# Kernel tuning notes

Hardware: AMD Instinct MI355X
Metric: run time of the kernel (lower is better)

The kernel has to match this reference:

```python
import jax, jax.numpy as jnp
import numpy as np

B, S, IN, H, C = 4, 1024, 1024, 256, 8

def setup_inputs() -> dict:
    key = jax.random.key(0)
    ks = jax.random.split(key, 9)
    scale_in = 1.0 / np.sqrt(IN)
    scale_h2 = 1.0 / np.sqrt(2 * H)
    return {
        "seq_feats": jax.random.normal(ks[0], (B, S, IN), dtype=jnp.float32),
        "U": jax.random.normal(ks[1], (H, C, H), dtype=jnp.float32) * 0.02,
        "W_weight": jax.random.uniform(ks[2], (C, 2 * H), minval=-scale_h2, maxval=scale_h2, dtype=jnp.float32),
        "W_bias": jax.random.uniform(ks[3], (C,), minval=-scale_h2, maxval=scale_h2, dtype=jnp.float32),
        "start_w": jax.random.uniform(ks[4], (H, IN), minval=-scale_in, maxval=scale_in, dtype=jnp.float32),
        "start_b": jax.random.uniform(ks[5], (H,), minval=-scale_in, maxval=scale_in, dtype=jnp.float32),
        "end_w": jax.random.uniform(ks[6], (H, IN), minval=-scale_in, maxval=scale_in, dtype=jnp.float32),
        "end_b": jax.random.uniform(ks[7], (H,), minval=-scale_in, maxval=scale_in, dtype=jnp.float32),
    }

def reference(seq_feats, U, W_weight, W_bias, start_w, start_b, end_w, end_b):
    # Hs, He: [b, s, h]
    Hs = jnp.einsum('bsi,hi->bsh', seq_feats, start_w) + start_b
    He = jnp.einsum('bsi,hi->bsh', seq_feats, end_w) + end_b
    # biaffine: [b, s, e, c]
    biaff = jnp.einsum('bsh,hcg,beg->bsec', Hs, U, He)
    # Linear over concat([Hs_repeat, He_repeat]) == split-weight broadcast sum
    Ws, We = W_weight[:, :256], W_weight[:, 256:]
    lin = (jnp.einsum('bsh,ch->bsc', Hs, Ws)[:, :, None, :]
           + jnp.einsum('beh,ch->bec', He, We)[:, None, :, :]
           + W_bias)
    return biaff + lin
```

## Files before the change

kernel.cpp:

```cpp
#include <hip/hip_runtime.h>
#include <stdint.h>


#define BDIM 256

typedef float f32x4 __attribute__((ext_vector_type(4)));
typedef __bf16 bf16x8 __attribute__((ext_vector_type(8)));
typedef unsigned int u32;
typedef unsigned short u16;
typedef const __attribute__((address_space(1))) u32* gas_ptr;
typedef __attribute__((address_space(3))) u32* las_ptr;

static __device__ __forceinline__ void load_lds16(const void* g, void* l) {
  __builtin_amdgcn_global_load_lds((gas_ptr)g, (las_ptr)l, 16, 0, 0);
}

static __device__ __forceinline__ u16 f32_to_bf16(float f) {
  union { float f; u32 u; } v; v.f = f;
  u32 r = v.u + 0x7FFFu + ((v.u >> 16) & 1u);
  return (u16)(r >> 16);
}
static __device__ __forceinline__ float bf16lo_to_f32(u32 u) {
  union { u32 u; float f; } v; v.u = u << 16;
  return v.f;
}
static __device__ __forceinline__ float bf16hi_to_f32(u32 u) {
  union { u32 u; float f; } v; v.u = u & 0xFFFF0000u;
  return v.f;
}

#define K3_LDSA(b) ((b) * 32768)
#define K3_LDSB(b) ((b) * 32768 + 16384)

#define STG(dstofs, src, srow, ld, kt)                                         \
  load_lds16((src) + (size_t)((srow) + (tid >> 3)) * (ld) + (kt) +             \
                 (((tid & 7) ^ ((tid >> 3) & 7)) << 3),                        \
             &lds[(dstofs) + tid * 8])

#define STG_A(b, mh, t) do {                                                   \
    STG(K3_LDSA(b) + (mh) * 4096,       Ag, m0 + (mh) * 64,       256, (t)*64);\
    STG(K3_LDSA(b) + ((mh)+2) * 4096,   Ag, m0 + 128 + (mh) * 64, 256, (t)*64);\
  } while (0)

#define STG_B(b, h, t) do {                                                    \
    STG(K3_LDSB(b) + (2*(h)) * 4096,    Bgz, n0 + (h) * 128,      512, (t)*64);\
    STG(K3_LDSB(b) + (2*(h)+1) * 4096,  Bgz, n0 + (h) * 128 + 64, 512, (t)*64);\
  } while (0)

#define RD_A(b, mh)                                                            \
  _Pragma("unroll")                                                            \
  for (int mi = 0; mi < 4; ++mi) {                                             \
    const int r = wr * 128 + (mh) * 64 + mi * 16 + rA;                         \
    _Pragma("unroll")                                                          \
    for (int ks = 0; ks < 2; ++ks)                                             \
      aF[mi][ks] = *reinterpret_cast<const bf16x8*>(                           \
          &lds[K3_LDSA(b) + r * 64 + ((((ks << 2) | kq) ^ (rA & 7)) << 3)]);   \
  }

#define RD_B(b)                                                                \
  _Pragma("unroll")                                                            \
  for (int nh = 0; nh < 2; ++nh)                                               \
  _Pragma("unroll")                                                            \
  for (int ni = 0; ni < 2; ++ni) {                                             \
    const int r = wc * 64 + nh * 32 + ni * 16 + rA;                            \
    _Pragma("unroll")                                                          \
    for (int ks = 0; ks < 2; ++ks)                                             \
      bF[nh][ni][ks] = *reinterpret_cast<const bf16x8*>(                       \
          &lds[K3_LDSB(b) + r * 64 + ((((ks << 2) | kq) ^ (rA & 7)) << 3)]);   \
  }

#define MFMA_Q(mh, nh)                                                         \
  __builtin_amdgcn_s_setprio(1);                                               \
  _Pragma("unroll")                                                            \
  for (int mi = 0; mi < 4; ++mi)                                               \
  _Pragma("unroll")                                                            \
  for (int ni = 0; ni < 2; ++ni)                                               \
  _Pragma("unroll")                                                            \
  for (int ks = 0; ks < 2; ++ks)                                               \
    acc[(mh)*4 + mi][(nh)*2 + ni] = __builtin_amdgcn_mfma_f32_16x16x32_bf16(   \
        aF[mi][ks], bF[nh][ni][ks], acc[(mh)*4 + mi][(nh)*2 + ni], 0, 0, 0);   \
  __builtin_amdgcn_s_setprio(0);

#define BARRIER_MID()                                                          \
  __builtin_amdgcn_sched_barrier(0);                                           \
  __builtin_amdgcn_s_barrier();                                                \
  asm volatile("s_waitcnt lgkmcnt(0)" ::: "memory");                           \
  __builtin_amdgcn_sched_barrier(0)

#define BARRIER_END()                                                          \
  __builtin_amdgcn_sched_barrier(0);                                           \
  __builtin_amdgcn_s_barrier()

__global__ __launch_bounds__(512, 2)
void gemm256_biaff(const u16* __restrict__ Tall,
                   const u16* __restrict__ Bg,
                   float* __restrict__ Out,
                   const float* __restrict__ linSall,
                   const float* __restrict__ linEall)
{
  extern __shared__ u16 lds[];

  const int tid  = threadIdx.x;
  const int lane = tid & 63;
  const int wv   = tid >> 6;
  const int wr   = wv >> 2;
  const int wc   = wv & 3;
  const int rA   = lane & 15;
  const int kq   = lane >> 4;
  const int z    = blockIdx.z;

  int id = blockIdx.y * gridDim.x + blockIdx.x;
  id = (id & 7) * 16 + (id >> 3);
  const int n0 = (id & 3) * 256;
  const int m0 = (id >> 2) * 256;

  const u16* Ag  = Tall + (size_t)z * (8192 * 256);
  const u16* Bgz = Bg   + (size_t)z * (1024 * 512);

  f32x4 acc[8][4];
#pragma unroll
  for (int i = 0; i < 8; ++i)
#pragma unroll
    for (int j = 0; j < 4; ++j) acc[i][j] = (f32x4)0.f;

  bf16x8 aF[4][2];
  bf16x8 bF[2][2][2];

  STG_A(0, 0, 0); STG_A(0, 1, 0); STG_B(0, 0, 0); STG_B(0, 1, 0);
  STG_A(1, 0, 1);
  asm volatile("s_waitcnt vmcnt(2)" ::: "memory");
  __builtin_amdgcn_s_barrier();

  constexpr int NT = 4;
#pragma unroll
  for (int i = 0; i < NT / 2; ++i) {
    const int t1 = 2 * i + 1, t2 = 2 * i + 2, t3 = 2 * i + 3;
    RD_A(0, 0); RD_B(0);
    STG_A(1, 1, t1);
    BARRIER_MID();
    MFMA_Q(0, 0);
    BARRIER_END();
    STG_B(1, 0, t1);
    BARRIER_MID();
    MFMA_Q(0, 1);
    BARRIER_END();
    RD_A(0, 1);
    STG_B(1, 1, t1);
    BARRIER_MID();
    MFMA_Q(1, 1);
    BARRIER_END();
    if (t2 < NT) {
      STG_A(0, 0, t2);
      asm volatile("s_waitcnt vmcnt(2)" ::: "memory");
    } else {
      asm volatile("s_waitcnt vmcnt(0)" ::: "memory");
    }
    BARRIER_MID();
    MFMA_Q(1, 0);
    BARRIER_END();
    RD_A(1, 0); RD_B(1);
    if (t2 < NT) STG_A(0, 1, t2);
    BARRIER_MID();
    MFMA_Q(0, 0);
    BARRIER_END();
    if (t2 < NT) STG_B(0, 0, t2);
    BARRIER_MID();
    MFMA_Q(0, 1);
    BARRIER_END();
    RD_A(1, 1);
    if (t2 < NT) STG_B(0, 1, t2);
    BARRIER_MID();
    MFMA_Q(1, 1);
    BARRIER_END();
    if (t3 < NT) {
      STG_A(1, 0, t3);
      asm volatile("s_waitcnt vmcnt(2)" ::: "memory");
    } else {
      asm volatile("s_waitcnt vmcnt(0)" ::: "memory");
    }
    BARRIER_MID();
    MFMA_Q(1, 0);
    BARRIER_END();
  }

  const int rgr = kq * 4;
  float* OutZ = Out + (size_t)z * 8388608;
  const float* lS = linSall + (size_t)z * 8192;
  const float* lE = linEall + (size_t)z * 8192;
#pragma unroll
  for (int mf = 0; mf < 8; ++mf) {
#pragma unroll
    for (int nf = 0; nf < 4; ++nf) {
      const int mBase = m0 + wr * 128 + mf * 16 + rgr;
      const int e = n0 + wc * 64 + (nf >> 1) * 32 + (nf & 1) * 16 + rA;
      const int s = mBase >> 3;
      const int c0 = mBase & 7;
      const float4 ls4 = *reinterpret_cast<const float4*>(lS + mBase);
      const float4 le4 = *reinterpret_cast<const float4*>(lE + (e << 3) + c0);
      float4 o;
      o.x = acc[mf][nf][0] + ls4.x + le4.x;
      o.y = acc[mf][nf][1] + ls4.y + le4.y;
      o.z = acc[mf][nf][2] + ls4.z + le4.z;
      o.w = acc[mf][nf][3] + ls4.w + le4.w;
      *reinterpret_cast<float4*>(OutZ + ((size_t)s << 13) + ((size_t)e << 3) + c0) = o;
    }
  }
}

template <int IM, int EPI>
__global__ __launch_bounds__(BDIM, 2)
void gemm_bt(const u16* __restrict__ Aall,
             const u16* __restrict__ Ball,
             void* __restrict__ OutAll,
             const int N, const int K, const int lda, const int ldb,
             const float* __restrict__ bias0,
             const float* __restrict__ bias1)
{
  constexpr int WM = IM * 16;
  constexpr int TM = 2 * WM;

  __shared__ u16 lsA[TM * 32];
  __shared__ u16 lsB[128 * 32];

  const int tid  = threadIdx.x;
  const int lane = tid & 63;
  const int wv   = tid >> 6;
  const int wr   = wv >> 1;
  const int wc   = wv & 1;

  const int gx = gridDim.x;
  const int nwg = gx * gridDim.y;
  int id = blockIdx.y * gx + blockIdx.x;
  {
    const int q = nwg >> 3;
    id = (id & 7) * q + (id >> 3);
  }
  const int n0 = (id % gx) * 128;
  const int m0 = (id / gx) * TM;

  const u16* A  = Aall;
  const u16* Bm = Ball;

  f32x4 acc[IM][4];
#pragma unroll
  for (int i = 0; i < IM; ++i)
#pragma unroll
    for (int j = 0; j < 4; ++j) acc[i][j] = (f32x4)0.f;

  const int rA = lane & 15;
  const int ko = (lane >> 4) * 8;

  for (int kt = 0; kt < K; kt += 32) {
    constexpr int CA = TM * 4;
#pragma unroll
    for (int it = 0; it < CA / BDIM; ++it) {
      const int chunk = it * BDIM + tid;
      const int row = chunk >> 2;
      const int ce = (chunk & 3) * 8;
      load_lds16(A + (size_t)(m0 + row) * lda + (kt + ce), &lsA[chunk * 8]);
    }
#pragma unroll
    for (int it = 0; it < 2; ++it) {
      const int chunk = it * BDIM + tid;
      const int row = chunk >> 2;
      const int ce = (chunk & 3) * 8;
      load_lds16(Bm + (size_t)(n0 + row) * ldb + (kt + ce), &lsB[chunk * 8]);
    }
    __syncthreads();

    bf16x8 aF[IM], bF[4];
#pragma unroll
    for (int i = 0; i < IM; ++i)
      aF[i] = *reinterpret_cast<const bf16x8*>(&lsA[(wr * WM + i * 16 + rA) * 32 + ko]);
#pragma unroll
    for (int j = 0; j < 4; ++j)
      bF[j] = *reinterpret_cast<const bf16x8*>(&lsB[(wc * 64 + j * 16 + rA) * 32 + ko]);
#pragma unroll
    for (int i = 0; i < IM; ++i)
#pragma unroll
      for (int j = 0; j < 4; ++j)
        acc[i][j] = __builtin_amdgcn_mfma_f32_16x16x32_bf16(aF[i], bF[j], acc[i][j], 0, 0, 0);
    __syncthreads();
  }

  const int rgr = (lane >> 4) * 4;
  u16* Out = (u16*)OutAll;
#pragma unroll
  for (int i = 0; i < IM; ++i) {
#pragma unroll
    for (int j = 0; j < 4; ++j) {
      const int mBase = m0 + wr * WM + i * 16 + rgr;
      const int n = n0 + wc * 64 + j * 16 + rA;
      float bn = 0.f;
      if constexpr (EPI == 1) bn = (n < 256) ? bias0[n] : bias1[n - 256];
#pragma unroll
      for (int r = 0; r < 4; ++r) {
        Out[(size_t)(mBase + r) * N + n] = f32_to_bf16(acc[i][j][r] + bn);
      }
    }
  }
}

__global__ void prep_kernel(const float* __restrict__ seq,
                            const float* __restrict__ sw,
                            const float* __restrict__ ew,
                            const float* __restrict__ U,
                            u16* __restrict__ Xbf,
                            u16* __restrict__ wbf,
                            u16* __restrict__ Ut)
{
  const int bid = blockIdx.x;
  const int tid = threadIdx.x;
  if (bid < 4096) {
    const int i = bid * 1024 + tid * 4;
    const float4 v = *reinterpret_cast<const float4*>(seq + i);
    ushort4 o;
    o.x = f32_to_bf16(v.x); o.y = f32_to_bf16(v.y);
    o.z = f32_to_bf16(v.z); o.w = f32_to_bf16(v.w);
    *reinterpret_cast<ushort4*>(Xbf + i) = o;
  } else if (bid < 4608) {
    const int i = (bid - 4096) * 1024 + tid * 4;
    const float* src = (i < 262144) ? (sw + i) : (ew + (i - 262144));
    const float4 v = *reinterpret_cast<const float4*>(src);
    ushort4 o;
    o.x = f32_to_bf16(v.x); o.y = f32_to_bf16(v.y);
    o.z = f32_to_bf16(v.z); o.w = f32_to_bf16(v.w);
    *reinterpret_cast<ushort4*>(wbf + i) = o;
  } else {
    const int i = (bid - 4608) * 1024 + tid * 4;
    const int n = i >> 8;
    const int h = i & 255;
    ushort4 o;
    o.x = f32_to_bf16(U[(size_t)(h + 0) * 2048 + n]);
    o.y = f32_to_bf16(U[(size_t)(h + 1) * 2048 + n]);
    o.z = f32_to_bf16(U[(size_t)(h + 2) * 2048 + n]);
    o.w = f32_to_bf16(U[(size_t)(h + 3) * 2048 + n]);
    *reinterpret_cast<ushort4*>(Ut + i) = o;
  }
}

__global__ void lin_kernel(const u16* __restrict__ Hboth,
                           const float* __restrict__ Ww,
                           const float* __restrict__ Wb,
                           float* __restrict__ linS,
                           float* __restrict__ linE)
{
  const int idx = blockIdx.x * BDIM + threadIdx.x;
  if (idx >= 4096 * 8) return;
  const int m = idx >> 3;
  const int c = idx & 7;
  const uint4* hs4 = reinterpret_cast<const uint4*>(Hboth + (size_t)m * 512);
  const uint4* he4 = reinterpret_cast<const uint4*>(Hboth + (size_t)m * 512 + 256);
  const float* ws = Ww + c * 512;
  const float* we = ws + 256;
  float s1 = 0.f, s2 = 0.f;
#pragma unroll 4
  for (int t = 0; t < 32; ++t) {
    const uint4 a = hs4[t];
    const uint4 b = he4[t];
    const u32 aw[4] = {a.x, a.y, a.z, a.w};
    const u32 bw[4] = {b.x, b.y, b.z, b.w};
#pragma unroll
    for (int q = 0; q < 4; ++q) {
      const int h = t * 8 + q * 2;
      s1 += bf16lo_to_f32(aw[q]) * ws[h] + bf16hi_to_f32(aw[q]) * ws[h + 1];
      s2 += bf16lo_to_f32(bw[q]) * we[h] + bf16hi_to_f32(bw[q]) * we[h + 1];
    }
  }
  linS[idx] = s1;
  linE[idx] = s2 + Wb[c];
}

extern "C" void kernel_launch(void* const* d_in, const int* in_sizes, int n_in,
                              void* d_out, int out_size, void* d_ws, size_t ws_size,
                              hipStream_t stream)
{
  const float* seq = (const float*)d_in[0];
  const float* U   = (const float*)d_in[1];
  const float* Ww  = (const float*)d_in[2];
  const float* Wb  = (const float*)d_in[3];
  const float* sw  = (const float*)d_in[4];
  const float* sb  = (const float*)d_in[5];
  const float* ew  = (const float*)d_in[6];
  const float* eb  = (const float*)d_in[7];
  float* out = (float*)d_out;

  u16* Xbf   = (u16*)d_ws;
  u16* wbf   = Xbf  + 4194304;
  u16* Utbf  = wbf  + 524288;
  u16* Hboth = Utbf + 524288;
  u16* Tbf   = Hboth + 2097152;
  float* linS = (float*)(Tbf + 8388608);
  float* linE = linS + 32768;

  prep_kernel<<<5120, BDIM, 0, stream>>>(seq, sw, ew, U, Xbf, wbf, Utbf);

  gemm_bt<2, 1><<<dim3(4, 64, 1), BDIM, 0, stream>>>(
      Xbf, wbf, Hboth, 512, 1024, 1024, 1024, sb, eb);

  lin_kernel<<<128, BDIM, 0, stream>>>(Hboth, Ww, Wb, linS, linE);

  gemm_bt<4, 0><<<dim3(16, 32, 1), BDIM, 0, stream>>>(
      Hboth, Utbf, Tbf, 2048, 256, 512, 256, nullptr, nullptr);

  hipFuncSetAttribute(reinterpret_cast<const void*>(&gemm256_biaff),
                      hipFuncAttributeMaxDynamicSharedMemorySize, 131072);
  gemm256_biaff<<<dim3(4, 32, 4), 512, 131072, stream>>>(
      Tbf, Hboth + 256, out, linS, linE);
}
```

Before: 97.33 us.

## Fuse all stages into one cooperative persistent kernel with grid syncs

```diff
diff --git a/kernel.cpp b/kernel.cpp
--- a/kernel.cpp
+++ b/kernel.cpp
@@ -1,8 +1,9 @@
 #include <hip/hip_runtime.h>
+#include <hip/hip_cooperative_groups.h>
 #include <stdint.h>
 
-
-#define BDIM 256
+namespace cg = cooperative_groups;
+
 
 typedef float f32x4 __attribute__((ext_vector_type(4)));
 typedef __bf16 bf16x8 __attribute__((ext_vector_type(8)));
@@ -29,346 +30,365 @@
   return v.f;
 }
 
+static __device__ __forceinline__ void stage64(u16* lds, int dst, const u16* src,
+                                               int srow, int ld, int kcol, int tid) {
+  const int r = tid >> 3;
+  const int sl = tid & 7;
+  load_lds16(src + (size_t)(srow + r) * ld + kcol + ((sl ^ (r & 7)) << 3),
+             &lds[dst + tid * 8]);
+}
+
+static __device__ __forceinline__ bf16x8 rd64(const u16* lds, int base, int row, int kslot) {
+  return *reinterpret_cast<const bf16x8*>(&lds[base + row * 64 + ((kslot ^ (row & 7)) << 3)]);
+}
+
 #define K3_LDSA(b) ((b) * 32768)
 #define K3_LDSB(b) ((b) * 32768 + 16384)
 
-#define STG(dstofs, src, srow, ld, kt)                                         \
-  load_lds16((src) + (size_t)((srow) + (tid >> 3)) * (ld) + (kt) +             \
-                 (((tid & 7) ^ ((tid >> 3) & 7)) << 3),                        \
-             &lds[(dstofs) + tid * 8])
-
-#define STG_A(b, mh, t) do {                                                   \
-    STG(K3_LDSA(b) + (mh) * 4096,       Ag, m0 + (mh) * 64,       256, (t)*64);\
-    STG(K3_LDSA(b) + ((mh)+2) * 4096,   Ag, m0 + 128 + (mh) * 64, 256, (t)*64);\
+#define STG_A(b, mh, t) do {                                                    \
+    stage64(lds, K3_LDSA(b) + (mh) * 4096,     Ag, m0 + (mh) * 64,       256, (t) * 64, tid); \
+    stage64(lds, K3_LDSA(b) + ((mh)+2) * 4096, Ag, m0 + 128 + (mh) * 64, 256, (t) * 64, tid); \
   } while (0)
 
-#define STG_B(b, h, t) do {                                                    \
-    STG(K3_LDSB(b) + (2*(h)) * 4096,    Bgz, n0 + (h) * 128,      512, (t)*64);\
-    STG(K3_LDSB(b) + (2*(h)+1) * 4096,  Bgz, n0 + (h) * 128 + 64, 512, (t)*64);\
+#define STG_B(b, h, t) do {                                                     \
+    stage64(lds, K3_LDSB(b) + (2*(h)) * 4096,   Bgz, n0 + (h) * 128,      512, (t) * 64, tid); \
+    stage64(lds, K3_LDSB(b) + (2*(h)+1) * 4096, Bgz, n0 + (h) * 128 + 64, 512, (t) * 64, tid); \
   } while (0)
 
-#define RD_A(b, mh)                                                            \
-  _Pragma("unroll")                                                            \
-  for (int mi = 0; mi < 4; ++mi) {                                             \
-    const int r = wr * 128 + (mh) * 64 + mi * 16 + rA;                         \
-    _Pragma("unroll")                                                          \
-    for (int ks = 0; ks < 2; ++ks)                                             \
-      aF[mi][ks] = *reinterpret_cast<const bf16x8*>(                           \
-          &lds[K3_LDSA(b) + r * 64 + ((((ks << 2) | kq) ^ (rA & 7)) << 3)]);   \
-  }
-
-#define RD_B(b)                                                                \
-  _Pragma("unroll")                                                            \
-  for (int nh = 0; nh < 2; ++nh)                                               \
-  _Pragma("unroll")                                                            \
-  for (int ni = 0; ni < 2; ++ni) {                                             \
-    const int r = wc * 64 + nh * 32 + ni * 16 + rA;                            \
-    _Pragma("unroll")                                                          \
-    for (int ks = 0; ks < 2; ++ks)                                             \
-      bF[nh][ni][ks] = *reinterpret_cast<const bf16x8*>(                       \
-          &lds[K3_LDSB(b) + r * 64 + ((((ks << 2) | kq) ^ (rA & 7)) << 3)]);   \
-  }
-
-#define MFMA_Q(mh, nh)                                                         \
-  __builtin_amdgcn_s_setprio(1);                                               \
-  _Pragma("unroll")                                                            \
-  for (int mi = 0; mi < 4; ++mi)                                               \
-  _Pragma("unroll")                                                            \
-  for (int ni = 0; ni < 2; ++ni)                                               \
-  _Pragma("unroll")                                                            \
-  for (int ks = 0; ks < 2; ++ks)                                               \
-    acc[(mh)*4 + mi][(nh)*2 + ni] = __builtin_amdgcn_mfma_f32_16x16x32_bf16(   \
-        aF[mi][ks], bF[nh][ni][ks], acc[(mh)*4 + mi][(nh)*2 + ni], 0, 0, 0);   \
+#define RD_A(b, mh)                                                             \
+  _Pragma("unroll")                                                             \
+  for (int mi = 0; mi < 4; ++mi)                                                \
+  _Pragma("unroll")                                                             \
+  for (int ks = 0; ks < 2; ++ks)                                                \
+    aF[mi][ks] = rd64(lds, K3_LDSA(b), wr * 128 + (mh) * 64 + mi * 16 + rA, (ks << 2) | kq);
+
+#define RD_B(b)                                                                 \
+  _Pragma("unroll")                                                             \
+  for (int nh = 0; nh < 2; ++nh)                                                \
+  _Pragma("unroll")                                                             \
+  for (int ni = 0; ni < 2; ++ni)                                                \
+  _Pragma("unroll")                                                             \
+  for (int ks = 0; ks < 2; ++ks)                                                \
+    bF[nh][ni][ks] = rd64(lds, K3_LDSB(b), wc * 64 + nh * 32 + ni * 16 + rA, (ks << 2) | kq);
+
+#define MFMA_Q(mh, nh)                                                          \
+  __builtin_amdgcn_s_setprio(1);                                                \
+  _Pragma("unroll")                                                             \
+  for (int mi = 0; mi < 4; ++mi)                                                \
+  _Pragma("unroll")                                                             \
+  for (int ni = 0; ni < 2; ++ni)                                                \
+  _Pragma("unroll")                                                             \
+  for (int ks = 0; ks < 2; ++ks)                                                \
+    acc[(mh)*4 + mi][(nh)*2 + ni] = __builtin_amdgcn_mfma_f32_16x16x32_bf16(    \
+        aF[mi][ks], bF[nh][ni][ks], acc[(mh)*4 + mi][(nh)*2 + ni], 0, 0, 0);    \
   __builtin_amdgcn_s_setprio(0);
 
-#define BARRIER_MID()                                                          \
-  __builtin_amdgcn_sched_barrier(0);                                           \
-  __builtin_amdgcn_s_barrier();                                                \
-  asm volatile("s_waitcnt lgkmcnt(0)" ::: "memory");                           \
+#define BARRIER_MID()                                                           \
+  __builtin_amdgcn_sched_barrier(0);                                            \
+  __builtin_amdgcn_s_barrier();                                                 \
+  asm volatile("s_waitcnt lgkmcnt(0)" ::: "memory");                            \
   __builtin_amdgcn_sched_barrier(0)
 
-#define BARRIER_END()                                                          \
-  __builtin_amdgcn_sched_barrier(0);                                           \
+#define BARRIER_END()                                                           \
+  __builtin_amdgcn_sched_barrier(0);                                            \
   __builtin_amdgcn_s_barrier()
 
 __global__ __launch_bounds__(512, 2)
-void gemm256_biaff(const u16* __restrict__ Tall,
-                   const u16* __restrict__ Bg,
-                   float* __restrict__ Out,
-                   const float* __restrict__ linSall,
-                   const float* __restrict__ linEall)
+void mega(const float* __restrict__ seq, const float* __restrict__ U,
+          const float* __restrict__ Ww, const float* __restrict__ Wb,
+          const float* __restrict__ sw, const float* __restrict__ sb,
+          const float* __restrict__ ew, const float* __restrict__ eb,
+          u16* __restrict__ ws, float* __restrict__ out)
 {
   extern __shared__ u16 lds[];
+  cg::grid_group gg = cg::this_grid();
+
+  u16* Xbf   = ws;
+  u16* wbf   = Xbf + 4194304;
+  u16* Utbf  = wbf + 524288;
+  u16* Hboth = Utbf + 524288;
+  u16* Tbf   = Hboth + 2097152;
+  float* linS = (float*)(Tbf + 8388608);
+  float* linE = linS + 32768;
 
   const int tid  = threadIdx.x;
+  const int bid  = blockIdx.x;
+  const int gtid = bid * 512 + tid;
   const int lane = tid & 63;
   const int wv   = tid >> 6;
-  const int wr   = wv >> 2;
-  const int wc   = wv & 3;
   const int rA   = lane & 15;
   const int kq   = lane >> 4;
-  const int z    = blockIdx.z;
-
-  int id = blockIdx.y * gridDim.x + blockIdx.x;
-  id = (id & 7) * 16 + (id >> 3);
-  const int n0 = (id & 3) * 256;
-  const int m0 = (id >> 2) * 256;
-
-  const u16* Ag  = Tall + (size_t)z * (8192 * 256);
-  const u16* Bgz = Bg   + (size_t)z * (1024 * 512);
-
-  f32x4 acc[8][4];
-#pragma unroll
-  for (int i = 0; i < 8; ++i)
-#pragma unroll
-    for (int j = 0; j < 4; ++j) acc[i][j] = (f32x4)0.f;
-
-  bf16x8 aF[4][2];
-  bf16x8 bF[2][2][2];
-
-  STG_A(0, 0, 0); STG_A(0, 1, 0); STG_B(0, 0, 0); STG_B(0, 1, 0);
-  STG_A(1, 0, 1);
-  asm volatile("s_waitcnt vmcnt(2)" ::: "memory");
-  __builtin_amdgcn_s_barrier();
-
-  constexpr int NT = 4;
-#pragma unroll
-  for (int i = 0; i < NT / 2; ++i) {
-    const int t1 = 2 * i + 1, t2 = 2 * i + 2, t3 = 2 * i + 3;
-    RD_A(0, 0); RD_B(0);
-    STG_A(1, 1, t1);
-    BARRIER_MID();
-    MFMA_Q(0, 0);
-    BARRIER_END();
-    STG_B(1, 0, t1);
-    BARRIER_MID();
-    MFMA_Q(0, 1);
-    BARRIER_END();
-    RD_A(0, 1);
-    STG_B(1, 1, t1);
-    BARRIER_MID();
-    MFMA_Q(1, 1);
-    BARRIER_END();
-    if (t2 < NT) {
-      STG_A(0, 0, t2);
+
+  {
+#pragma unroll
+    for (int kk = 0; kk < 8; ++kk) {
+      const int i = (gtid + kk * 131072) * 4;
+      const float4 v = *reinterpret_cast<const float4*>(seq + i);
+      ushort4 o;
+      o.x = f32_to_bf16(v.x); o.y = f32_to_bf16(v.y);
+      o.z = f32_to_bf16(v.z); o.w = f32_to_bf16(v.w);
+      *reinterpret_cast<ushort4*>(Xbf + i) = o;
+    }
+    {
+      const int i = gtid * 4;
+      const float* src = (i < 262144) ? (sw + i) : (ew + (i - 262144));
+      const float4 v = *reinterpret_cast<const float4*>(src);
+      ushort4 o;
+      o.x = f32_to_bf16(v.x); o.y = f32_to_bf16(v.y);
+      o.z = f32_to_bf16(v.z); o.w = f32_to_bf16(v.w);
+      *reinterpret_cast<ushort4*>(wbf + i) = o;
+    }
+    {
+      const int i = gtid * 4;
+      const int n = i >> 8;
+      const int h = i & 255;
+      ushort4 o;
+      o.x = f32_to_bf16(U[(size_t)(h + 0) * 2048 + n]);
+      o.y = f32_to_bf16(U[(size_t)(h + 1) * 2048 + n]);
+      o.z = f32_to_bf16(U[(size_t)(h + 2) * 2048 + n]);
+      o.w = f32_to_bf16(U[(size_t)(h + 3) * 2048 + n]);
+      *reinterpret_cast<ushort4*>(Utbf + i) = o;
+    }
+  }
+  __threadfence();
+  gg.sync();
+
+  {
+    const int wr = wv >> 2;
+    const int wc = wv & 3;
+    const int m0 = (bid >> 2) * 64;
+    const int n0 = (bid & 3) * 128;
+    f32x4 a1[2][2];
+#pragma unroll
+    for (int i = 0; i < 2; ++i)
+#pragma unroll
+      for (int j = 0; j < 2; ++j) a1[i][j] = (f32x4)0.f;
+
+    for (int kt = 0; kt < 1024; kt += 64) {
+      stage64(lds, 0,    Xbf, m0,      1024, kt, tid);
+      stage64(lds, 4096, wbf, n0,      1024, kt, tid);
+      stage64(lds, 8192, wbf, n0 + 64, 1024, kt, tid);
+      __syncthreads();
+      bf16x8 af[2][2], bfr[2][2];
+#pragma unroll
+      for (int mi = 0; mi < 2; ++mi)
+#pragma unroll
+        for (int ks = 0; ks < 2; ++ks)
+          af[mi][ks] = rd64(lds, 0, wr * 32 + mi * 16 + rA, (ks << 2) | kq);
+#pragma unroll
+      for (int ni = 0; ni < 2; ++ni)
+#pragma unroll
+        for (int ks = 0; ks < 2; ++ks)
+          bfr[ni][ks] = rd64(lds, 4096, wc * 32 + ni * 16 + rA, (ks << 2) | kq);
+#pragma unroll
+      for (int mi = 0; mi < 2; ++mi)
+#pragma unroll
+        for (int ni = 0; ni < 2; ++ni)
+#pragma unroll
+          for (int ks = 0; ks < 2; ++ks)
+            a1[mi][ni] = __builtin_amdgcn_mfma_f32_16x16x32_bf16(
+                af[mi][ks], bfr[ni][ks], a1[mi][ni], 0, 0, 0);
+      __syncthreads();
+    }
+#pragma unroll
+    for (int mi = 0; mi < 2; ++mi)
+#pragma unroll
+      for (int ni = 0; ni < 2; ++ni) {
+        const int n = n0 + wc * 32 + ni * 16 + rA;
+        const float bn = (n < 256) ? sb[n] : eb[n - 256];
+        const int mr = m0 + wr * 32 + mi * 16 + kq * 4;
+#pragma unroll
+        for (int r = 0; r < 4; ++r)
+          Hboth[(size_t)(mr + r) * 512 + n] = f32_to_bf16(a1[mi][ni][r] + bn);
+      }
+  }
+  __threadfence();
+  gg.sync();
+
+  if (gtid < 32768) {
+    const int m = gtid >> 3;
+    const int c = gtid & 7;
+    const uint4* hs4 = reinterpret_cast<const uint4*>(Hboth + (size_t)m * 512);
+    const uint4* he4 = reinterpret_cast<const uint4*>(Hboth + (size_t)m * 512 + 256);
+    const float* wsp = Ww + c * 512;
+    const float* wep = wsp + 256;
+    float s1 = 0.f, s2 = 0.f;
+#pragma unroll 4
+    for (int t = 0; t < 32; ++t) {
+      const uint4 a = hs4[t];
+      const uint4 b = he4[t];
+      const u32 aw[4] = {a.x, a.y, a.z, a.w};
+      const u32 bw[4] = {b.x, b.y, b.z, b.w};
+#pragma unroll
+      for (int q = 0; q < 4; ++q) {
+        const int h = t * 8 + q * 2;
+        s1 += bf16lo_to_f32(aw[q]) * wsp[h] + bf16hi_to_f32(aw[q]) * wsp[h + 1];
+        s2 += bf16lo_to_f32(bw[q]) * wep[h] + bf16hi_to_f32(bw[q]) * wep[h + 1];
+      }
+    }
+    linS[gtid] = s1;
+    linE[gtid] = s2 + Wb[c];
+  }
+  {
+    const int wr = wv >> 2;
+    const int wc = wv & 3;
+#pragma unroll 1
+    for (int rep = 0; rep < 2; ++rep) {
+      const int tile = bid + rep * 256;
+      const int m0 = (tile >> 4) * 128;
+      const int n0 = (tile & 15) * 128;
+      f32x4 a2[4][2];
+#pragma unroll
+      for (int i = 0; i < 4; ++i)
+#pragma unroll
+        for (int j = 0; j < 2; ++j) a2[i][j] = (f32x4)0.f;
+
+      for (int kt = 0; kt < 256; kt += 64) {
+        stage64(lds, 0,     Hboth, m0,       512, kt, tid);
+        stage64(lds, 4096,  Hboth, m0 + 64,  512, kt, tid);
+        stage64(lds, 8192,  Utbf,  n0,       256, kt, tid);
+        stage64(lds, 12288, Utbf,  n0 + 64,  256, kt, tid);
+        __syncthreads();
+        bf16x8 af[4][2], bfr[2][2];
+#pragma unroll
+        for (int mi = 0; mi < 4; ++mi)
+#pragma unroll
+          for (int ks = 0; ks < 2; ++ks)
+            af[mi][ks] = rd64(lds, 0, wr * 64 + mi * 16 + rA, (ks << 2) | kq);
+#pragma unroll
+        for (int ni = 0; ni < 2; ++ni)
+#pragma unroll
+          for (int ks = 0; ks < 2; ++ks)
+            bfr[ni][ks] = rd64(lds, 8192, wc * 32 + ni * 16 + rA, (ks << 2) | kq);
+#pragma unroll
+        for (int mi = 0; mi < 4; ++mi)
+#pragma unroll
+          for (int ni = 0; ni < 2; ++ni)
+#pragma unroll
+            for (int ks = 0; ks < 2; ++ks)
+              a2[mi][ni] = __builtin_amdgcn_mfma_f32_16x16x32_bf16(
+                  af[mi][ks], bfr[ni][ks], a2[mi][ni], 0, 0, 0);
+        __syncthreads();
+      }
+#pragma unroll
+      for (int mi = 0; mi < 4; ++mi)
+#pragma unroll
+        for (int ni = 0; ni < 2; ++ni) {
+          const int n = n0 + wc * 32 + ni * 16 + rA;
+          const int mr = m0 + wr * 64 + mi * 16 + kq * 4;
+#pragma unroll
+          for (int r = 0; r < 4; ++r)
+            Tbf[(size_t)(mr + r) * 2048 + n] = f32_to_bf16(a2[mi][ni][r]);
+        }
+    }
+  }
+  __threadfence();
+  gg.sync();
+
+  {
+    const int wr = wv >> 2;
+    const int wc = wv & 3;
+    f32x4 acc[8][4];
+    bf16x8 aF[4][2];
+    bf16x8 bF[2][2][2];
+#pragma unroll 1
+    for (int rep = 0; rep < 2; ++rep) {
+      const int tile = bid + rep * 256;
+      const int z = tile >> 7;
+      int id = tile & 127;
+      id = (id & 7) * 16 + (id >> 3);
+      const int n0 = (id & 3) * 256;
+      const int m0 = (id >> 2) * 256;
+
+      const u16* Ag  = Tbf + (size_t)z * (8192 * 256);
+      const u16* Bgz = Hboth + 256 + (size_t)z * (1024 * 512);
+
+#pragma unroll
+      for (int i = 0; i < 8; ++i)
+#pragma unroll
+        for (int j = 0; j < 4; ++j) acc[i][j] = (f32x4)0.f;
+
+      STG_A(0, 0, 0); STG_A(0, 1, 0); STG_B(0, 0, 0); STG_B(0, 1, 0);
+      STG_A(1, 0, 1);
       asm volatile("s_waitcnt vmcnt(2)" ::: "memory");
-    } else {
-      asm volatile("s_waitcnt vmcnt(0)" ::: "memory");
-    }
-    BARRIER_MID();
-    MFMA_Q(1, 0);
-    BARRIER_END();
-    RD_A(1, 0); RD_B(1);
-    if (t2 < NT) STG_A(0, 1, t2);
-    BARRIER_MID();
-    MFMA_Q(0, 0);
-    BARRIER_END();
-    if (t2 < NT) STG_B(0, 0, t2);
-    BARRIER_MID();
-    MFMA_Q(0, 1);
-    BARRIER_END();
-    RD_A(1, 1);
-    if (t2 < NT) STG_B(0, 1, t2);
-    BARRIER_MID();
-    MFMA_Q(1, 1);
-    BARRIER_END();
-    if (t3 < NT) {
-      STG_A(1, 0, t3);
-      asm volatile("s_waitcnt vmcnt(2)" ::: "memory");
-    } else {
-      asm volatile("s_waitcnt vmcnt(0)" ::: "memory");
-    }
-    BARRIER_MID();
-    MFMA_Q(1, 0);
-    BARRIER_END();
+      __builtin_amdgcn_s_barrier();
+
+      constexpr int NT = 4;
+#pragma unroll
+      for (int i = 0; i < NT / 2; ++i) {
+        const int t1 = 2 * i + 1, t2 = 2 * i + 2, t3 = 2 * i + 3;
+        RD_A(0, 0); RD_B(0);
+        STG_A(1, 1, t1);
+        BARRIER_MID();
+        MFMA_Q(0, 0);
+        BARRIER_END();
+        STG_B(1, 0, t1);
+        BARRIER_MID();
+        MFMA_Q(0, 1);
+        BARRIER_END();
+        RD_A(0, 1);
+        STG_B(1, 1, t1);
+        BARRIER_MID();
+        MFMA_Q(1, 1);
+        BARRIER_END();
+        if (t2 < NT) {
+          STG_A(0, 0, t2);
+          asm volatile("s_waitcnt vmcnt(2)" ::: "memory");
+        } else {
+          asm volatile("s_waitcnt vmcnt(0)" ::: "memory");
+        }
+        BARRIER_MID();
+        MFMA_Q(1, 0);
+        BARRIER_END();
+        RD_A(1, 0); RD_B(1);
+        if (t2 < NT) STG_A(0, 1, t2);
+        BARRIER_MID();
+        MFMA_Q(0, 0);
+        BARRIER_END();
+        if (t2 < NT) STG_B(0, 0, t2);
+        BARRIER_MID();
+        MFMA_Q(0, 1);
+        BARRIER_END();
+        RD_A(1, 1);
+        if (t2 < NT) STG_B(0, 1, t2);
+        BARRIER_MID();
+        MFMA_Q(1, 1);
+        BARRIER_END();
+        if (t3 < NT) {
+          STG_A(1, 0, t3);
+          asm volatile("s_waitcnt vmcnt(2)" ::: "memory");
+        } else {
+          asm volatile("s_waitcnt vmcnt(0)" ::: "memory");
+        }
+        BARRIER_MID();
+        MFMA_Q(1, 0);
+        BARRIER_END();
+      }
+
+      const int rgr = kq * 4;
+      float* OutZ = out + (size_t)z * 8388608;
+      const float* lS = linS + (size_t)z * 8192;
+      const float* lE = linE + (size_t)z * 8192;
+#pragma unroll
+      for (int mf = 0; mf < 8; ++mf) {
+#pragma unroll
+        for (int nf = 0; nf < 4; ++nf) {
+          const int mBase = m0 + wr * 128 + mf * 16 + rgr;
+          const int e = n0 + wc * 64 + (nf >> 1) * 32 + (nf & 1) * 16 + rA;
+          const int s = mBase >> 3;
+          const int c0 = mBase & 7;
+          const float4 ls4 = *reinterpret_cast<const float4*>(lS + mBase);
+          const float4 le4 = *reinterpret_cast<const float4*>(lE + (e << 3) + c0);
+          float4 o;
+          o.x = acc[mf][nf][0] + ls4.x + le4.x;
+          o.y = acc[mf][nf][1] + ls4.y + le4.y;
+          o.z = acc[mf][nf][2] + ls4.z + le4.z;
+          o.w = acc[mf][nf][3] + ls4.w + le4.w;
+          *reinterpret_cast<float4*>(OutZ + ((size_t)s << 13) + ((size_t)e << 3) + c0) = o;
+        }
+      }
+    }
   }
-
-  const int rgr = kq * 4;
-  float* OutZ = Out + (size_t)z * 8388608;
-  const float* lS = linSall + (size_t)z * 8192;
-  const float* lE = linEall + (size_t)z * 8192;
-#pragma unroll
-  for (int mf = 0; mf < 8; ++mf) {
-#pragma unroll
-    for (int nf = 0; nf < 4; ++nf) {
-      const int mBase = m0 + wr * 128 + mf * 16 + rgr;
-      const int e = n0 + wc * 64 + (nf >> 1) * 32 + (nf & 1) * 16 + rA;
-      const int s = mBase >> 3;
-      const int c0 = mBase & 7;
-      const float4 ls4 = *reinterpret_cast<const float4*>(lS + mBase);
-      const float4 le4 = *reinterpret_cast<const float4*>(lE + (e << 3) + c0);
-      float4 o;
-      o.x = acc[mf][nf][0] + ls4.x + le4.x;
-      o.y = acc[mf][nf][1] + ls4.y + le4.y;
-      o.z = acc[mf][nf][2] + ls4.z + le4.z;
-      o.w = acc[mf][nf][3] + ls4.w + le4.w;
-      *reinterpret_cast<float4*>(OutZ + ((size_t)s << 13) + ((size_t)e << 3) + c0) = o;
-    }
-  }
-}
-
-template <int IM, int EPI>
-__global__ __launch_bounds__(BDIM, 2)
-void gemm_bt(const u16* __restrict__ Aall,
-             const u16* __restrict__ Ball,
-             void* __restrict__ OutAll,
-             const int N, const int K, const int lda, const int ldb,
-             const float* __restrict__ bias0,
-             const float* __restrict__ bias1)
-{
-  constexpr int WM = IM * 16;
-  constexpr int TM = 2 * WM;
-
-  __shared__ u16 lsA[TM * 32];
-  __shared__ u16 lsB[128 * 32];
-
-  const int tid  = threadIdx.x;
-  const int lane = tid & 63;
-  const int wv   = tid >> 6;
-  const int wr   = wv >> 1;
-  const int wc   = wv & 1;
-
-  const int gx = gridDim.x;
-  const int nwg = gx * gridDim.y;
-  int id = blockIdx.y * gx + blockIdx.x;
-  {
-    const int q = nwg >> 3;
-    id = (id & 7) * q + (id >> 3);
-  }
-  const int n0 = (id % gx) * 128;
-  const int m0 = (id / gx) * TM;
-
-  const u16* A  = Aall;
-  const u16* Bm = Ball;
-
-  f32x4 acc[IM][4];
-#pragma unroll
-  for (int i = 0; i < IM; ++i)
-#pragma unroll
-    for (int j = 0; j < 4; ++j) acc[i][j] = (f32x4)0.f;
-
-  const int rA = lane & 15;
-  const int ko = (lane >> 4) * 8;
-
-  for (int kt = 0; kt < K; kt += 32) {
-    constexpr int CA = TM * 4;
-#pragma unroll
-    for (int it = 0; it < CA / BDIM; ++it) {
-      const int chunk = it * BDIM + tid;
-      const int row = chunk >> 2;
-      const int ce = (chunk & 3) * 8;
-      load_lds16(A + (size_t)(m0 + row) * lda + (kt + ce), &lsA[chunk * 8]);
-    }
-#pragma unroll
-    for (int it = 0; it < 2; ++it) {
-      const int chunk = it * BDIM + tid;
-      const int row = chunk >> 2;
-      const int ce = (chunk & 3) * 8;
-      load_lds16(Bm + (size_t)(n0 + row) * ldb + (kt + ce), &lsB[chunk * 8]);
-    }
-    __syncthreads();
-
-    bf16x8 aF[IM], bF[4];
-#pragma unroll
-    for (int i = 0; i < IM; ++i)
-      aF[i] = *reinterpret_cast<const bf16x8*>(&lsA[(wr * WM + i * 16 + rA) * 32 + ko]);
-#pragma unroll
-    for (int j = 0; j < 4; ++j)
-      bF[j] = *reinterpret_cast<const bf16x8*>(&lsB[(wc * 64 + j * 16 + rA) * 32 + ko]);
-#pragma unroll
-    for (int i = 0; i < IM; ++i)
-#pragma unroll
-      for (int j = 0; j < 4; ++j)
-        acc[i][j] = __builtin_amdgcn_mfma_f32_16x16x32_bf16(aF[i], bF[j], acc[i][j], 0, 0, 0);
-    __syncthreads();
-  }
-
-  const int rgr = (lane >> 4) * 4;
-  u16* Out = (u16*)OutAll;
-#pragma unroll
-  for (int i = 0; i < IM; ++i) {
-#pragma unroll
-    for (int j = 0; j < 4; ++j) {
-      const int mBase = m0 + wr * WM + i * 16 + rgr;
-      const int n = n0 + wc * 64 + j * 16 + rA;
-      float bn = 0.f;
-      if constexpr (EPI == 1) bn = (n < 256) ? bias0[n] : bias1[n - 256];
-#pragma unroll
-      for (int r = 0; r < 4; ++r) {
-        Out[(size_t)(mBase + r) * N + n] = f32_to_bf16(acc[i][j][r] + bn);
-      }
-    }
-  }
-}
-
-__global__ void prep_kernel(const float* __restrict__ seq,
-                            const float* __restrict__ sw,
-                            const float* __restrict__ ew,
-                            const float* __restrict__ U,
-                            u16* __restrict__ Xbf,
-                            u16* __restrict__ wbf,
-                            u16* __restrict__ Ut)
-{
-  const int bid = blockIdx.x;
-  const int tid = threadIdx.x;
-  if (bid < 4096) {
-    const int i = bid * 1024 + tid * 4;
-    const float4 v = *reinterpret_cast<const float4*>(seq + i);
-    ushort4 o;
-    o.x = f32_to_bf16(v.x); o.y = f32_to_bf16(v.y);
-    o.z = f32_to_bf16(v.z); o.w = f32_to_bf16(v.w);
-    *reinterpret_cast<ushort4*>(Xbf + i) = o;
-  } else if (bid < 4608) {
-    const int i = (bid - 4096) * 1024 + tid * 4;
-    const float* src = (i < 262144) ? (sw + i) : (ew + (i - 262144));
-    const float4 v = *reinterpret_cast<const float4*>(src);
-    ushort4 o;
-    o.x = f32_to_bf16(v.x); o.y = f32_to_bf16(v.y);
-    o.z = f32_to_bf16(v.z); o.w = f32_to_bf16(v.w);
-    *reinterpret_cast<ushort4*>(wbf + i) = o;
-  } else {
-    const int i = (bid - 4608) * 1024 + tid * 4;
-    const int n = i >> 8;
-    const int h = i & 255;
-    ushort4 o;
-    o.x = f32_to_bf16(U[(size_t)(h + 0) * 2048 + n]);
-    o.y = f32_to_bf16(U[(size_t)(h + 1) * 2048 + n]);
-    o.z = f32_to_bf16(U[(size_t)(h + 2) * 2048 + n]);
-    o.w = f32_to_bf16(U[(size_t)(h + 3) * 2048 + n]);
-    *reinterpret_cast<ushort4*>(Ut + i) = o;
-  }
-}
-
-__global__ void lin_kernel(const u16* __restrict__ Hboth,
-                           const float* __restrict__ Ww,
-                           const float* __restrict__ Wb,
-                           float* __restrict__ linS,
-                           float* __restrict__ linE)
-{
-  const int idx = blockIdx.x * BDIM + threadIdx.x;
-  if (idx >= 4096 * 8) return;
-  const int m = idx >> 3;
-  const int c = idx & 7;
-  const uint4* hs4 = reinterpret_cast<const uint4*>(Hboth + (size_t)m * 512);
-  const uint4* he4 = reinterpret_cast<const uint4*>(Hboth + (size_t)m * 512 + 256);
-  const float* ws = Ww + c * 512;
-  const float* we = ws + 256;
-  float s1 = 0.f, s2 = 0.f;
-#pragma unroll 4
-  for (int t = 0; t < 32; ++t) {
-    const uint4 a = hs4[t];
-    const uint4 b = he4[t];
-    const u32 aw[4] = {a.x, a.y, a.z, a.w};
-    const u32 bw[4] = {b.x, b.y, b.z, b.w};
-#pragma unroll
-    for (int q = 0; q < 4; ++q) {
-      const int h = t * 8 + q * 2;
-      s1 += bf16lo_to_f32(aw[q]) * ws[h] + bf16hi_to_f32(aw[q]) * ws[h + 1];
-      s2 += bf16lo_to_f32(bw[q]) * we[h] + bf16hi_to_f32(bw[q]) * we[h + 1];
-    }
-  }
-  linS[idx] = s1;
-  linE[idx] = s2 + Wb[c];
 }
 
 extern "C" void kernel_launch(void* const* d_in, const int* in_sizes, int n_in,
@@ -384,27 +404,14 @@
   const float* ew  = (const float*)d_in[6];
   const float* eb  = (const float*)d_in[7];
   float* out = (float*)d_out;
-
-  u16* Xbf   = (u16*)d_ws;
-  u16* wbf   = Xbf  + 4194304;
-  u16* Utbf  = wbf  + 524288;
-  u16* Hboth = Utbf + 524288;
-  u16* Tbf   = Hboth + 2097152;
-  float* linS = (float*)(Tbf + 8388608);
-  float* linE = linS + 32768;
-
-  prep_kernel<<<5120, BDIM, 0, stream>>>(seq, sw, ew, U, Xbf, wbf, Utbf);
-
-  gemm_bt<2, 1><<<dim3(4, 64, 1), BDIM, 0, stream>>>(
-      Xbf, wbf, Hboth, 512, 1024, 1024, 1024, sb, eb);
-
-  lin_kernel<<<128, BDIM, 0, stream>>>(Hboth, Ww, Wb, linS, linE);
-
-  gemm_bt<4, 0><<<dim3(16, 32, 1), BDIM, 0, stream>>>(
-      Hboth, Utbf, Tbf, 2048, 256, 512, 256, nullptr, nullptr);
-
-  hipFuncSetAttribute(reinterpret_cast<const void*>(&gemm256_biaff),
+  u16* ws16 = (u16*)d_ws;
+
+  hipFuncSetAttribute(reinterpret_cast<const void*>(&mega),
                       hipFuncAttributeMaxDynamicSharedMemorySize, 131072);
-  gemm256_biaff<<<dim3(4, 32, 4), 512, 131072, stream>>>(
-      Tbf, Hboth + 256, out, linS, linE);
-}
+
+  void* args[] = {(void*)&seq, (void*)&U,  (void*)&Ww, (void*)&Wb,
+                  (void*)&sw,  (void*)&sb, (void*)&ew, (void*)&eb,
+                  (void*)&ws16, (void*)&out};
+  hipLaunchCooperativeKernel(reinterpret_cast<void*>(&mega),
+                             dim3(256), dim3(512), args, 131072, stream);
+}
```

New measurement: 365.7 us. +275.8%, slower.
